# Optimization experiments

Hardware: AMD Instinct MI355X
Metric: run time of the kernel (lower is better)

Reference implementation:

```python
import jax, jax.numpy as jnp
import numpy as np

B, N, M, C = 2, 8192, 1024, 1152  # batch, dense points, centers, feature dim
K = 3                              # three_nn interpolation
EPS = 1e-8


def setup_inputs() -> dict:
    key = jax.random.key(0)
    k1, k2, k3 = jax.random.split(key, 3)
    xyz = jax.random.normal(k1, (B, N, 3), dtype=jnp.float32)      # query points
    center = jax.random.normal(k2, (B, M, 3), dtype=jnp.float32)   # center coords (already permuted to B,M,3)
    feats = jax.random.normal(k3, (B, C, M), dtype=jnp.float32)    # backbone features at centers
    return {"xyz": xyz, "center": center, "feats": feats}


def _interpolate(xyz, center, feats):
    # Squared pairwise distances [B, N, M] (PointNet++ three_nn uses squared dists).
    d2 = (jnp.sum(xyz * xyz, axis=-1, keepdims=True)
          + jnp.sum(center * center, axis=-1)[:, None, :]
          - 2.0 * jnp.einsum('bnd,bmd->bnm', xyz, center))
    neg_top, idx = jax.lax.top_k(-d2, K)          # 3 nearest centers per point
    dist = -neg_top                                # [B, N, K] squared distances
    recip = 1.0 / (dist + EPS)
    weight = recip / jnp.sum(recip, axis=-1, keepdims=True)  # [B, N, K]
    fm = jnp.transpose(feats, (0, 2, 1))           # [B, M, C]
    batch_idx = jnp.arange(B)[:, None, None]       # broadcast gather over batch
    gathered = fm[batch_idx, idx]                  # [B, N, K, C]
    out = jnp.einsum('bnkc,bnk->bcn', gathered, weight)  # [B, C, N]
    return out


def reference(xyz, center, feats):
    return _interpolate(xyz, center, feats)
```

## Files before the change

kernel.cpp:

```cpp
#include <hip/hip_runtime.h>
#include <cstdint>

#define B_ 2
#define N_ 8192
#define M_ 1024
#define C_ 1152
#define EPS_ 1e-8f
#define NT 32
#define CHUNK 128
#define NBN (N_ / NT)
#define NBC (C_ / CHUNK)
#define PTS 16
#define NSL 2
#define MSL (M_ / NSL)
#define NNB ((N_ / PTS) * NSL * B_)
#define TRB ((M_ / 64) * (C_ / 64) * B_)

typedef float f32x4 __attribute__((ext_vector_type(4)));

__device__ __forceinline__ unsigned short f2bf(float f) {
    unsigned u = __float_as_uint(f);
    u += 0x7fffu + ((u >> 16) & 1u);
    return (unsigned short)(u >> 16);
}
__device__ __forceinline__ float bf2f(unsigned short h) {
    return __uint_as_float(((unsigned)h) << 16);
}

__device__ __forceinline__ void ins3lex(float d, int i,
        float& d0, int& i0, float& d1, int& i1, float& d2, int& i2) {
    bool b0 = (d < d0) || (d == d0 && i < i0);
    bool b1 = (d < d1) || (d == d1 && i < i1);
    bool b2 = (d < d2) || (d == d2 && i < i2);
    d2 = b1 ? d1 : (b2 ? d : d2);   i2 = b1 ? i1 : (b2 ? i : i2);
    d1 = b0 ? d0 : (b1 ? d : d1);   i1 = b0 ? i0 : (b1 ? i : i1);
    d0 = b0 ? d  : d0;              i0 = b0 ? i  : i0;
}

__global__ __launch_bounds__(256) void k_front(const float* __restrict__ feats,
                                               unsigned short* __restrict__ fm,
                                               const float* __restrict__ xyz,
                                               const float* __restrict__ center,
                                               float* __restrict__ cand) {
    __shared__ float4 shb[1040];
    int bid = blockIdx.x;
    int t   = threadIdx.x;

    if (bid >= NNB) {
        float* tile = (float*)shb;
        int tb = bid - NNB;
        int within = tb % ((M_ / 64) * (C_ / 64));
        int b  = tb / ((M_ / 64) * (C_ / 64));
        int mb = within & 15;
        int cb = within >> 4;
        int m0 = mb * 64;
        int c0 = cb * 64;
        int tx = t & 63;
        int ty = t >> 6;
        const float* src = feats + ((size_t)b * C_ + c0) * M_ + m0;
#pragma unroll
        for (int j = 0; j < 16; ++j) {
            int cl = ty + 4 * j;
            tile[cl * 65 + tx] = __builtin_nontemporal_load(&src[(size_t)cl * M_ + tx]);
        }
        __syncthreads();
        unsigned short* dst = fm + ((size_t)b * M_ + m0) * C_ + c0;
#pragma unroll
        for (int j = 0; j < 16; ++j) {
            int ml = ty + 4 * j;
            dst[(size_t)ml * C_ + tx] = f2bf(tile[tx * 65 + ml]);
        }
        return;
    }

    float4* sc = shb;
    int b      = bid >> 10;
    int within = bid & 1023;
    int pg     = within >> 1;
    int s      = within & 1;
    int n0     = pg * PTS;
    int msl    = s * MSL;

    {
        int i0s = 2 * t;
        const float* cp = center + ((size_t)b * M_ + msl + i0s) * 3;
        float ax = cp[0], ay = cp[1], az = cp[2];
        float bx = cp[3], by = cp[4], bz = cp[5];
        float acc = __fadd_rn(__fadd_rn(__fmul_rn(ax, ax), __fmul_rn(ay, ay)),
                              __fmul_rn(az, az));
        float bcc = __fadd_rn(__fadd_rn(__fmul_rn(bx, bx), __fmul_rn(by, by)),
                              __fmul_rn(bz, bz));
        sc[i0s]     = make_float4(ax, ay, az, acc);
        sc[i0s + 1] = make_float4(bx, by, bz, bcc);
    }
    __syncthreads();

    int p = t >> 4;
    int c = t & 15;
    int n = n0 + p;
    float x = xyz[((size_t)b * N_ + n) * 3 + 0];
    float y = xyz[((size_t)b * N_ + n) * 3 + 1];
    float z = xyz[((size_t)b * N_ + n) * 3 + 2];
    float xx = __fadd_rn(__fadd_rn(__fmul_rn(x, x), __fmul_rn(y, y)),
                         __fmul_rn(z, z));

    float d0 = __builtin_inff(), d1 = __builtin_inff(), d2 = __builtin_inff();
    int   i0 = 0x7fffffff,  i1 = 0x7fffffff,  i2 = 0x7fffffff;
#pragma unroll 8
    for (int it = 0; it < MSL / 16; ++it) {
        float4 v = sc[c + it * 16];
        float dot = __fmaf_rn(z, v.z, __fmaf_rn(y, v.y, __fmul_rn(x, v.x)));
        float s0  = __fadd_rn(xx, v.w);
        float d   = __fmaf_rn(-2.0f, dot, s0);
        int   m   = msl + c + it * 16;
        bool b0 = d < d0;
        bool b1 = d < d1;
        bool b2 = d < d2;
        float nd0 = fminf(d, d0);
        float nd1 = __builtin_amdgcn_fmed3f(d, d0, d1);
        float nd2 = __builtin_amdgcn_fmed3f(d, d1, d2);
        i2 = b1 ? i1 : (b2 ? m : i2);
        i1 = b0 ? i0 : (b1 ? m : i1);
        i0 = b0 ? m  : i0;
        d0 = nd0; d1 = nd1; d2 = nd2;
    }

#pragma unroll
    for (int off = 1; off <= 8; off <<= 1) {
        float e0 = __shfl_xor(d0, off); int j0 = __shfl_xor(i0, off);
        float e1 = __shfl_xor(d1, off); int j1 = __shfl_xor(i1, off);
        float e2 = __shfl_xor(d2, off); int j2 = __shfl_xor(i2, off);
        ins3lex(e0, j0, d0, i0, d1, i1, d2, i2);
        ins3lex(e1, j1, d0, i0, d1, i1, d2, i2);
        ins3lex(e2, j2, d0, i0, d1, i1, d2, i2);
    }
    if (c == 0) {
        size_t base = (((size_t)b * N_ + n) * NSL + s) * 6;
        cand[base + 0] = d0; ((int*)cand)[base + 1] = i0;
        cand[base + 2] = d1; ((int*)cand)[base + 3] = i1;
        cand[base + 4] = d2; ((int*)cand)[base + 5] = i2;
    }
}

__global__ __launch_bounds__(256) void k_interp(const unsigned short* __restrict__ fm,
                                                const float* __restrict__ cand,
                                                float* __restrict__ out) {
    __shared__ float T[NT][CHUNK + 1];
    __shared__ int   sbase[NT][3];
    __shared__ float sw[NT][3];
    int flat = blockIdx.x;
    int slot = flat & 7;
    int b    = slot >> 2;
    int idx  = (flat >> 3) * 4 + (slot & 3);
    int n0   = (idx & (NBN - 1)) * NT;
    int c0   = (idx >> 8) * CHUNK;
    int t    = threadIdx.x;
    if (t < NT) {
        size_t cb = ((size_t)b * N_ + n0 + t) * (NSL * 6);
        float D0 = cand[cb + 0]; int I0 = ((const int*)cand)[cb + 1];
        float D1 = cand[cb + 2]; int I1 = ((const int*)cand)[cb + 3];
        float D2 = cand[cb + 4]; int I2 = ((const int*)cand)[cb + 5];
        ins3lex(cand[cb + 6],  ((const int*)cand)[cb + 7],  D0, I0, D1, I1, D2, I2);
        ins3lex(cand[cb + 8],  ((const int*)cand)[cb + 9],  D0, I0, D1, I1, D2, I2);
        ins3lex(cand[cb + 10], ((const int*)cand)[cb + 11], D0, I0, D1, I1, D2, I2);
        float r0 = 1.0f / __fadd_rn(D0, EPS_);
        float r1 = 1.0f / __fadd_rn(D1, EPS_);
        float r2 = 1.0f / __fadd_rn(D2, EPS_);
        float s  = __fadd_rn(__fadd_rn(r0, r1), r2);
        sbase[t][0] = (b * M_ + I0) * C_;  sw[t][0] = r0 / s;
        sbase[t][1] = (b * M_ + I1) * C_;  sw[t][1] = r1 / s;
        sbase[t][2] = (b * M_ + I2) * C_;  sw[t][2] = r2 / s;
    }
    __syncthreads();
    int wave = t >> 6;
    int lane = t & 63;
    int half = lane >> 5;
    int cl   = (lane & 31) * 4;
#pragma unroll
    for (int pp = 0; pp < 4; ++pp) {
        int p = pp * 8 + wave * 2 + half;
        float w0 = sw[p][0], w1 = sw[p][1], w2 = sw[p][2];
        const ushort4 a0 = *(const ushort4*)(fm + sbase[p][0] + c0 + cl);
        const ushort4 a1 = *(const ushort4*)(fm + sbase[p][1] + c0 + cl);
        const ushort4 a2 = *(const ushort4*)(fm + sbase[p][2] + c0 + cl);
        T[p][cl + 0] = __fmaf_rn(bf2f(a2.x), w2, __fmaf_rn(bf2f(a1.x), w1, __fmul_rn(bf2f(a0.x), w0)));
        T[p][cl + 1] = __fmaf_rn(bf2f(a2.y), w2, __fmaf_rn(bf2f(a1.y), w1, __fmul_rn(bf2f(a0.y), w0)));
        T[p][cl + 2] = __fmaf_rn(bf2f(a2.z), w2, __fmaf_rn(bf2f(a1.z), w1, __fmul_rn(bf2f(a0.z), w0)));
        T[p][cl + 3] = __fmaf_rn(bf2f(a2.w), w2, __fmaf_rn(bf2f(a1.w), w1, __fmul_rn(bf2f(a0.w), w0)));
    }
    __syncthreads();
    int p4  = (t & 7) * 4;
    int ccb = t >> 3;
#pragma unroll
    for (int r = 0; r < 4; ++r) {
        int cc = r * 32 + ccb;
        f32x4 v = { T[p4 + 0][cc], T[p4 + 1][cc], T[p4 + 2][cc], T[p4 + 3][cc] };
        __builtin_nontemporal_store(v,
            (f32x4*)&out[((size_t)b * C_ + c0 + cc) * N_ + n0 + p4]);
    }
}

extern "C" void kernel_launch(void* const* d_in, const int* in_sizes, int n_in,
                              void* d_out, int out_size, void* d_ws, size_t ws_size,
                              hipStream_t stream) {
    const float* xyz    = (const float*)d_in[0];
    const float* center = (const float*)d_in[1];
    const float* feats  = (const float*)d_in[2];
    float* out = (float*)d_out;

    char*           ws   = (char*)d_ws;
    unsigned short* fm   = (unsigned short*)ws;
    float*          cand = (float*)(ws + (size_t)B_ * M_ * C_ * 2);

    k_front <<<NNB + TRB, 256, 0, stream>>>(feats, fm, xyz, center, cand);
    k_interp<<<NBN * NBC * B_, 256, 0, stream>>>(fm, cand, out);
}
```

Baseline: 36.01 us.

## Process two query points per thread and split centers into four slices

The kNN stage now splits the centers into four slices of 256 instead of two of 512, and each thread tracks two query points that share every center value loaded from LDS. The block count stays the same, and each thread's loop is shorter and fully unrolled. Reading each center once for two points reduces LDS traffic per distance, and the extra independent chains raise instruction-level parallelism. In exchange, register pressure and shuffle-merge work double, and the interp kernel must merge four candidate sets per point instead of two.

```diff
diff --git a/kernel.cpp b/kernel.cpp
--- a/kernel.cpp
+++ b/kernel.cpp
@@ -10,8 +10,8 @@
 #define CHUNK 128
 #define NBN (N_ / NT)
 #define NBC (C_ / CHUNK)
-#define PTS 16
-#define NSL 2
+#define PTS 32
+#define NSL 4
 #define MSL (M_ / NSL)
 #define NNB ((N_ / PTS) * NSL * B_)
 #define TRB ((M_ / 64) * (C_ / 64) * B_)
@@ -76,69 +76,95 @@
     float4* sc = shb;
     int b      = bid >> 10;
     int within = bid & 1023;
-    int pg     = within >> 1;
-    int s      = within & 1;
+    int pg     = within >> 2;
+    int s      = within & 3;
     int n0     = pg * PTS;
     int msl    = s * MSL;
 
     {
-        int i0s = 2 * t;
-        const float* cp = center + ((size_t)b * M_ + msl + i0s) * 3;
+        const float* cp = center + ((size_t)b * M_ + msl + t) * 3;
         float ax = cp[0], ay = cp[1], az = cp[2];
-        float bx = cp[3], by = cp[4], bz = cp[5];
         float acc = __fadd_rn(__fadd_rn(__fmul_rn(ax, ax), __fmul_rn(ay, ay)),
                               __fmul_rn(az, az));
-        float bcc = __fadd_rn(__fadd_rn(__fmul_rn(bx, bx), __fmul_rn(by, by)),
-                              __fmul_rn(bz, bz));
-        sc[i0s]     = make_float4(ax, ay, az, acc);
-        sc[i0s + 1] = make_float4(bx, by, bz, bcc);
+        sc[t] = make_float4(ax, ay, az, acc);
     }
     __syncthreads();
 
-    int p = t >> 4;
-    int c = t & 15;
-    int n = n0 + p;
-    float x = xyz[((size_t)b * N_ + n) * 3 + 0];
-    float y = xyz[((size_t)b * N_ + n) * 3 + 1];
-    float z = xyz[((size_t)b * N_ + n) * 3 + 2];
-    float xx = __fadd_rn(__fadd_rn(__fmul_rn(x, x), __fmul_rn(y, y)),
-                         __fmul_rn(z, z));
-
-    float d0 = __builtin_inff(), d1 = __builtin_inff(), d2 = __builtin_inff();
-    int   i0 = 0x7fffffff,  i1 = 0x7fffffff,  i2 = 0x7fffffff;
-#pragma unroll 8
+    int pp = t >> 4;
+    int c  = t & 15;
+    int nA = n0 + pp;
+    int nB = n0 + pp + 16;
+    const float* xpA = xyz + ((size_t)b * N_ + nA) * 3;
+    const float* xpB = xyz + ((size_t)b * N_ + nB) * 3;
+    float xA = xpA[0], yA = xpA[1], zA = xpA[2];
+    float xB = xpB[0], yB = xpB[1], zB = xpB[2];
+    float xxA = __fadd_rn(__fadd_rn(__fmul_rn(xA, xA), __fmul_rn(yA, yA)),
+                          __fmul_rn(zA, zA));
+    float xxB = __fadd_rn(__fadd_rn(__fmul_rn(xB, xB), __fmul_rn(yB, yB)),
+                          __fmul_rn(zB, zB));
+
+    float dA0 = __builtin_inff(), dA1 = __builtin_inff(), dA2 = __builtin_inff();
+    int   iA0 = 0x7fffffff,  iA1 = 0x7fffffff,  iA2 = 0x7fffffff;
+    float dB0 = __builtin_inff(), dB1 = __builtin_inff(), dB2 = __builtin_inff();
+    int   iB0 = 0x7fffffff,  iB1 = 0x7fffffff,  iB2 = 0x7fffffff;
+#pragma unroll
     for (int it = 0; it < MSL / 16; ++it) {
         float4 v = sc[c + it * 16];
-        float dot = __fmaf_rn(z, v.z, __fmaf_rn(y, v.y, __fmul_rn(x, v.x)));
-        float s0  = __fadd_rn(xx, v.w);
-        float d   = __fmaf_rn(-2.0f, dot, s0);
-        int   m   = msl + c + it * 16;
-        bool b0 = d < d0;
-        bool b1 = d < d1;
-        bool b2 = d < d2;
-        float nd0 = fminf(d, d0);
-        float nd1 = __builtin_amdgcn_fmed3f(d, d0, d1);
-        float nd2 = __builtin_amdgcn_fmed3f(d, d1, d2);
-        i2 = b1 ? i1 : (b2 ? m : i2);
-        i1 = b0 ? i0 : (b1 ? m : i1);
-        i0 = b0 ? m  : i0;
-        d0 = nd0; d1 = nd1; d2 = nd2;
+        int   m  = msl + c + it * 16;
+        {
+            float dot = __fmaf_rn(zA, v.z, __fmaf_rn(yA, v.y, __fmul_rn(xA, v.x)));
+            float d   = __fmaf_rn(-2.0f, dot, __fadd_rn(xxA, v.w));
+            bool b0 = d < dA0;
+            bool b1 = d < dA1;
+            bool b2 = d < dA2;
+            float nd0 = fminf(d, dA0);
+            float nd1 = __builtin_amdgcn_fmed3f(d, dA0, dA1);
+            float nd2 = __builtin_amdgcn_fmed3f(d, dA1, dA2);
+            iA2 = b1 ? iA1 : (b2 ? m : iA2);
+            iA1 = b0 ? iA0 : (b1 ? m : iA1);
+            iA0 = b0 ? m   : iA0;
+            dA0 = nd0; dA1 = nd1; dA2 = nd2;
+        }
+        {
+            float dot = __fmaf_rn(zB, v.z, __fmaf_rn(yB, v.y, __fmul_rn(xB, v.x)));
+            float d   = __fmaf_rn(-2.0f, dot, __fadd_rn(xxB, v.w));
+            bool b0 = d < dB0;
+            bool b1 = d < dB1;
+            bool b2 = d < dB2;
+            float nd0 = fminf(d, dB0);
+            float nd1 = __builtin_amdgcn_fmed3f(d, dB0, dB1);
+            float nd2 = __builtin_amdgcn_fmed3f(d, dB1, dB2);
+            iB2 = b1 ? iB1 : (b2 ? m : iB2);
+            iB1 = b0 ? iB0 : (b1 ? m : iB1);
+            iB0 = b0 ? m   : iB0;
+            dB0 = nd0; dB1 = nd1; dB2 = nd2;
+        }
     }
 
 #pragma unroll
     for (int off = 1; off <= 8; off <<= 1) {
-        float e0 = __shfl_xor(d0, off); int j0 = __shfl_xor(i0, off);
-        float e1 = __shfl_xor(d1, off); int j1 = __shfl_xor(i1, off);
-        float e2 = __shfl_xor(d2, off); int j2 = __shfl_xor(i2, off);
-        ins3lex(e0, j0, d0, i0, d1, i1, d2, i2);
-        ins3lex(e1, j1, d0, i0, d1, i1, d2, i2);
-        ins3lex(e2, j2, d0, i0, d1, i1, d2, i2);
+        float e0 = __shfl_xor(dA0, off); int j0 = __shfl_xor(iA0, off);
+        float e1 = __shfl_xor(dA1, off); int j1 = __shfl_xor(iA1, off);
+        float e2 = __shfl_xor(dA2, off); int j2 = __shfl_xor(iA2, off);
+        ins3lex(e0, j0, dA0, iA0, dA1, iA1, dA2, iA2);
+        ins3lex(e1, j1, dA0, iA0, dA1, iA1, dA2, iA2);
+        ins3lex(e2, j2, dA0, iA0, dA1, iA1, dA2, iA2);
+        float f0 = __shfl_xor(dB0, off); int k0 = __shfl_xor(iB0, off);
+        float f1 = __shfl_xor(dB1, off); int k1 = __shfl_xor(iB1, off);
+        float f2 = __shfl_xor(dB2, off); int k2 = __shfl_xor(iB2, off);
+        ins3lex(f0, k0, dB0, iB0, dB1, iB1, dB2, iB2);
+        ins3lex(f1, k1, dB0, iB0, dB1, iB1, dB2, iB2);
+        ins3lex(f2, k2, dB0, iB0, dB1, iB1, dB2, iB2);
     }
     if (c == 0) {
-        size_t base = (((size_t)b * N_ + n) * NSL + s) * 6;
-        cand[base + 0] = d0; ((int*)cand)[base + 1] = i0;
-        cand[base + 2] = d1; ((int*)cand)[base + 3] = i1;
-        cand[base + 4] = d2; ((int*)cand)[base + 5] = i2;
+        size_t baseA = (((size_t)b * N_ + nA) * NSL + s) * 6;
+        cand[baseA + 0] = dA0; ((int*)cand)[baseA + 1] = iA0;
+        cand[baseA + 2] = dA1; ((int*)cand)[baseA + 3] = iA1;
+        cand[baseA + 4] = dA2; ((int*)cand)[baseA + 5] = iA2;
+        size_t baseB = (((size_t)b * N_ + nB) * NSL + s) * 6;
+        cand[baseB + 0] = dB0; ((int*)cand)[baseB + 1] = iB0;
+        cand[baseB + 2] = dB1; ((int*)cand)[baseB + 3] = iB1;
+        cand[baseB + 4] = dB2; ((int*)cand)[baseB + 5] = iB2;
     }
 }
 
@@ -160,9 +186,13 @@
         float D0 = cand[cb + 0]; int I0 = ((const int*)cand)[cb + 1];
         float D1 = cand[cb + 2]; int I1 = ((const int*)cand)[cb + 3];
         float D2 = cand[cb + 4]; int I2 = ((const int*)cand)[cb + 5];
-        ins3lex(cand[cb + 6],  ((const int*)cand)[cb + 7],  D0, I0, D1, I1, D2, I2);
-        ins3lex(cand[cb + 8],  ((const int*)cand)[cb + 9],  D0, I0, D1, I1, D2, I2);
-        ins3lex(cand[cb + 10], ((const int*)cand)[cb + 11], D0, I0, D1, I1, D2, I2);
+#pragma unroll
+        for (int sl = 1; sl < NSL; ++sl) {
+            size_t sb = cb + sl * 6;
+            ins3lex(cand[sb + 0], ((const int*)cand)[sb + 1], D0, I0, D1, I1, D2, I2);
+            ins3lex(cand[sb + 2], ((const int*)cand)[sb + 3], D0, I0, D1, I1, D2, I2);
+            ins3lex(cand[sb + 4], ((const int*)cand)[sb + 5], D0, I0, D1, I1, D2, I2);
+        }
         float r0 = 1.0f / __fadd_rn(D0, EPS_);
         float r1 = 1.0f / __fadd_rn(D1, EPS_);
         float r2 = 1.0f / __fadd_rn(D2, EPS_);
```

Result: slower. 44.85 us (+24.5%).
